# Performance work log

Hardware: AMD Instinct MI355X
Metric: run time of the kernel (lower is better)

## Reference

```python
import jax, jax.numpy as jnp
import numpy as np


def setup_inputs() -> dict:
    key = jax.random.key(0)
    k_x, k_q, k_k, k_v = jax.random.split(key, 4)
    seq_len, d_in, d_out = 4096, 1024, 1024
    x = jax.random.normal(k_x, (seq_len, d_in), dtype=jnp.float32)
    # torch nn.Linear weights are [d_out, d_in]; applied as x @ W.T
    scale = 1.0 / np.sqrt(d_in)
    Wq = jax.random.uniform(k_q, (d_out, d_in), jnp.float32, -scale, scale)
    Wk = jax.random.uniform(k_k, (d_out, d_in), jnp.float32, -scale, scale)
    Wv = jax.random.uniform(k_v, (d_out, d_in), jnp.float32, -scale, scale)
    return {"x": x, "Wq": Wq, "Wk": Wk, "Wv": Wv}


def reference(x, Wq, Wk, Wv):
    # x: [S, d_in]; Wq/Wk/Wv: [d_out, d_in]
    queries = x @ Wq.T          # [S, d_out]
    keys = x @ Wk.T             # [S, d_out]
    values = x @ Wv.T           # [S, d_out]
    d_k = keys.shape[-1]
    attn_scores = queries @ keys.T                      # [S, S]
    attn_weights = jax.nn.softmax(attn_scores / jnp.sqrt(jnp.float32(d_k)), axis=-1)
    S = attn_scores.shape[0]
    tril = jnp.tril(jnp.ones((S, S), dtype=attn_weights.dtype))
    masked = tril * attn_weights
    masked_norm = masked / jnp.sum(masked, axis=-1, keepdims=True)
    context_vec = masked_norm @ values                  # [S, d_out]
    return context_vec
```

## Files before the change

kernel.cpp:

```cpp
#include <hip/hip_runtime.h>
#include <hip/hip_bf16.h>


typedef __bf16 bf16_t;
typedef __bf16 bf16x4v __attribute__((ext_vector_type(4)));
typedef __bf16 bf16x8 __attribute__((ext_vector_type(8)));
typedef float f32x4 __attribute__((ext_vector_type(4)));
typedef unsigned char u8;
typedef long long i64_t;

#define AS1 __attribute__((address_space(1)))
#define AS3 __attribute__((address_space(3)))

__device__ __forceinline__ void async_copy16(const void* g, void* l) {
    __builtin_amdgcn_global_load_lds((AS1 void*)(g), (AS3 void*)(l), 16, 0, 0);
}

__device__ __forceinline__ u8 f32_to_fp8(float v) {
    return (u8)(__builtin_amdgcn_cvt_pk_fp8_f32(v, v, 0, false) & 0xff);
}

__device__ __forceinline__ void store_conv(float* p, float v) { *p = v; }
__device__ __forceinline__ void store_conv(bf16_t* p, float v) { *p = (bf16_t)v; }
__device__ __forceinline__ void store_conv(u8* p, float v) { *p = f32_to_fp8(v); }

__device__ __forceinline__ float sum64(const float* p) {
    const f32x4* v = (const f32x4*)p;
    float s = 0.f;
#pragma unroll
    for (int u = 0; u < 16; ++u) {
        f32x4 a = v[u];
        s += a[0] + a[1] + a[2] + a[3];
    }
    return s;
}

template <int EPI, typename OutT>
__device__ __forceinline__ void gemm_tile_bf16(const bf16_t* __restrict__ A, int lda,
                                               const bf16_t* __restrict__ B, int ldb,
                                               OutT* __restrict__ C, int ldc,
                                               int kb0, int kb1, float alpha,
                                               bf16_t* __restrict__ As,
                                               bf16_t* __restrict__ Bs,
                                               const float* __restrict__ inv) {
    constexpr int BK = 64;
    const int tid = threadIdx.x;
    const int lane = tid & 63, wave = tid >> 6;
    const int wm = wave >> 1, wn = wave & 1;
    const int q = lane >> 4, l16 = lane & 15;

    f32x4 acc[4][4] = {};

    const bf16_t* aSrc[4];
    const bf16_t* bSrc[4];
    int ldsOff[4];
#pragma unroll
    for (int it = 0; it < 4; ++it) {
        int c = it * 256 + tid;
        int r = c >> 3, b = c & 7;
        int sb = b ^ (r & 7);
        aSrc[it] = A + (size_t)r * lda + sb * 8;
        bSrc[it] = B + (size_t)r * ldb + sb * 8;
        ldsOff[it] = c * 8;
    }

    for (int kb = kb0; kb < kb1; ++kb) {
        const int k0 = kb * BK;
#pragma unroll
        for (int it = 0; it < 4; ++it) async_copy16(aSrc[it] + k0, &As[ldsOff[it]]);
#pragma unroll
        for (int it = 0; it < 4; ++it) async_copy16(bSrc[it] + k0, &Bs[ldsOff[it]]);
        __syncthreads();

#pragma unroll
        for (int k2 = 0; k2 < 2; ++k2) {
            bf16x8 af[4], bfr[4];
#pragma unroll
            for (int mt = 0; mt < 4; ++mt) {
                int m = wm * 64 + mt * 16 + l16;
                int blk = (k2 * 4 + q) ^ (m & 7);
                af[mt] = *(const bf16x8*)&As[m * BK + blk * 8];
            }
#pragma unroll
            for (int nt = 0; nt < 4; ++nt) {
                int nn = wn * 64 + nt * 16 + l16;
                int blk = (k2 * 4 + q) ^ (nn & 7);
                bfr[nt] = *(const bf16x8*)&Bs[nn * BK + blk * 8];
            }
#pragma unroll
            for (int mt = 0; mt < 4; ++mt)
#pragma unroll
                for (int nt = 0; nt < 4; ++nt)
                    acc[mt][nt] = __builtin_amdgcn_mfma_f32_16x16x32_bf16(
                        af[mt], bfr[nt], acc[mt][nt], 0, 0, 0);
        }
        __syncthreads();
    }

    const int row0 = wm * 64, col0 = wn * 64;
#pragma unroll
    for (int mt = 0; mt < 4; ++mt)
#pragma unroll
        for (int nt = 0; nt < 4; ++nt)
#pragma unroll
            for (int r = 0; r < 4; ++r) {
                int lr = row0 + mt * 16 + q * 4 + r;
                float v = acc[mt][nt][r];
                v = (EPI == 2) ? v * inv[lr] : v * alpha;
                store_conv(&C[(size_t)lr * ldc + col0 + nt * 16 + l16], v);
            }
}

__device__ __forceinline__ void scores_tile_fp8(const u8* __restrict__ A, int lda,
                                                const u8* __restrict__ B, int ldb,
                                                bf16_t* __restrict__ C, int ldc,
                                                float alpha,
                                                u8* __restrict__ As, u8* __restrict__ Bs,
                                                float* __restrict__ partial,
                                                int gr0, int gc0,
                                                float* __restrict__ sred) {
    const int tid = threadIdx.x;
    const int lane = tid & 63, wave = tid >> 6;
    const int wm = wave >> 1, wn = wave & 1;
    const int q = lane >> 4, l16 = lane & 15;

    f32x4 acc[4][2] = {};

    const u8* aSrc[4];
    int aOff[4];
#pragma unroll
    for (int it = 0; it < 4; ++it) {
        int c = it * 256 + tid;
        int r = c >> 3, b = c & 7;
        int sb = b ^ (r & 7);
        aSrc[it] = A + (size_t)r * lda + sb * 16;
        aOff[it] = c * 16;
    }
    const u8* bSrc[2];
    int bOff[2];
#pragma unroll
    for (int it = 0; it < 2; ++it) {
        int c = it * 256 + tid;
        int r = c >> 3, b = c & 7;
        int sb = b ^ (r & 7);
        bSrc[it] = B + (size_t)r * ldb + sb * 16;
        bOff[it] = c * 16;
    }

    for (int kb = 0; kb < 8; ++kb) {
        const int k0 = kb * 128;
#pragma unroll
        for (int it = 0; it < 4; ++it) async_copy16(aSrc[it] + k0, &As[aOff[it]]);
#pragma unroll
        for (int it = 0; it < 2; ++it) async_copy16(bSrc[it] + k0, &Bs[bOff[it]]);
        __syncthreads();

#pragma unroll
        for (int k2 = 0; k2 < 4; ++k2) {
            i64_t af[4], bfr[2];
            const int cb = 2 * k2 + (q >> 1), co = (q & 1) * 8;
#pragma unroll
            for (int mt = 0; mt < 4; ++mt) {
                int m = wm * 64 + mt * 16 + l16;
                af[mt] = *(const i64_t*)&As[m * 128 + ((cb ^ (m & 7)) << 4) + co];
            }
#pragma unroll
            for (int nt = 0; nt < 2; ++nt) {
                int nn = wn * 32 + nt * 16 + l16;
                bfr[nt] = *(const i64_t*)&Bs[nn * 128 + ((cb ^ (nn & 7)) << 4) + co];
            }
#pragma unroll
            for (int mt = 0; mt < 4; ++mt)
#pragma unroll
                for (int nt = 0; nt < 2; ++nt)
                    acc[mt][nt] = __builtin_amdgcn_mfma_f32_16x16x32_fp8_fp8(
                        af[mt], bfr[nt], acc[mt][nt], 0, 0, 0);
        }
        __syncthreads();
    }

    const int row0 = wm * 64, col0 = wn * 32;
    float esum[4][4];
#pragma unroll
    for (int mt = 0; mt < 4; ++mt)
#pragma unroll
        for (int r = 0; r < 4; ++r) esum[mt][r] = 0.f;
#pragma unroll
    for (int mt = 0; mt < 4; ++mt)
#pragma unroll
        for (int nt = 0; nt < 2; ++nt)
#pragma unroll
            for (int r = 0; r < 4; ++r) {
                int lr = row0 + mt * 16 + q * 4 + r;
                int lc = col0 + nt * 16 + l16;
                float p = (gc0 + lc > gr0 + lr) ? 0.f : __expf(acc[mt][nt][r] * alpha);
                esum[mt][r] += p;
                C[(size_t)lr * ldc + lc] = (bf16_t)p;
            }
#pragma unroll
    for (int mt = 0; mt < 4; ++mt)
#pragma unroll
        for (int r = 0; r < 4; ++r) {
#pragma unroll
            for (int off = 1; off < 16; off <<= 1)
                esum[mt][r] += __shfl_xor(esum[mt][r], off, 64);
            if (l16 == 0) sred[(row0 + mt * 16 + q * 4 + r) * 2 + wn] = esum[mt][r];
        }
    __syncthreads();
    if (tid < 128) partial[(size_t)tid * 64] = sred[tid * 2] + sred[tid * 2 + 1];
}

__global__ __launch_bounds__(256) void k_qkv(const bf16_t* __restrict__ xb,
                                             const bf16_t* __restrict__ wqk,
                                             const bf16_t* __restrict__ wvb,
                                             u8* __restrict__ qk,
                                             bf16_t* __restrict__ vt) {
    __shared__ __attribute__((aligned(16))) bf16_t As[128 * 64];
    __shared__ __attribute__((aligned(16))) bf16_t Bs[128 * 64];
    int b = blockIdx.x;
    if (b < 512) {
        int bmi = b & 3, bn = (b >> 2) & 15, bmo = b >> 6;
        int bm = bmo * 4 + bmi;
        gemm_tile_bf16<0, u8>(xb + (size_t)bm * 128 * 1024, 1024,
                              wqk + (size_t)bn * 128 * 1024, 1024,
                              qk + (size_t)bm * 128 * 2048 + bn * 128, 2048,
                              0, 16, 1.f, As, Bs, nullptr);
    } else {
        int t = b - 512;
        int bm = t & 7, bn = t >> 3;
        gemm_tile_bf16<0, bf16_t>(wvb + (size_t)bm * 128 * 1024, 1024,
                                  xb + (size_t)bn * 128 * 1024, 1024,
                                  vt + (size_t)bm * 128 * 4096 + bn * 128, 4096,
                                  0, 16, 1.f, As, Bs, nullptr);
    }
}

__global__ __launch_bounds__(256) void k_scores(const u8* __restrict__ qk,
                                                bf16_t* __restrict__ P,
                                                float* __restrict__ rowsum_part) {
    __shared__ __attribute__((aligned(16))) u8 As[128 * 128];
    __shared__ __attribute__((aligned(16))) u8 Bs[64 * 128];
    __shared__ float sred[128 * 2];
    int t = blockIdx.x;
    int bm = (int)((sqrtf(4.f * (float)t + 1.f) - 1.f) * 0.5f);
    while (bm * bm + bm > t) --bm;
    while ((bm + 1) * (bm + 1) + (bm + 1) <= t) ++bm;
    int bn = t - bm * bm - bm;
    scores_tile_fp8(qk + (size_t)bm * 128 * 2048, 2048,
                    qk + 1024 + (size_t)bn * 64 * 2048, 2048,
                    P + (size_t)bm * 128 * 4096 + bn * 64, 4096,
                    0.03125f, As, Bs,
                    rowsum_part + (size_t)bm * 128 * 64 + bn,
                    bm * 128, bn * 64, sred);
    if (bn == 2 * bm + 1) {
        float* rp = rowsum_part + (size_t)bm * 128 * 64;
        int tid = threadIdx.x;
        for (int r = tid >> 4; r < 128; r += 16)
            for (int u = 2 * bm + 2 + (tid & 15); u < 64; u += 16)
                rp[r * 64 + u] = 0.f;
    }
}

__global__ __launch_bounds__(256) void k_pv(const bf16_t* __restrict__ P,
                                            const bf16_t* __restrict__ vt,
                                            const float* __restrict__ rowsum_part,
                                            float* __restrict__ out,
                                            float* __restrict__ partials) {
    __shared__ __attribute__((aligned(16))) bf16_t As[128 * 64];
    __shared__ __attribute__((aligned(16))) bf16_t Bs[128 * 64];
    __shared__ float sInv[128];
    int b = blockIdx.x;
    int bn = b & 7, g = b >> 3;
    int bm, s, ns;
    if (g < 8)       { bm = g;                 s = 0;            ns = 1; }
    else if (g < 24) { bm = 8 + (g - 8) / 2;   s = (g - 8) % 2;  ns = 2; }
    else if (g < 48) { bm = 16 + (g - 24) / 3; s = (g - 24) % 3; ns = 3; }
    else             { bm = 24 + (g - 48) / 4; s = (g - 48) % 4; ns = 4; }
    int nk = 2 * (bm + 1);
    int kb0 = s * nk / ns;
    int kb1 = (s + 1) * nk / ns;

    const bf16_t* A = P + (size_t)bm * 128 * 4096;
    const bf16_t* B = vt + (size_t)bn * 128 * 4096;
    if (ns == 1) {
        int tid = threadIdx.x;
        if (tid < 128)
            sInv[tid] = 1.f / sum64(rowsum_part + (size_t)(bm * 128 + tid) * 64);
        gemm_tile_bf16<2, float>(A, 4096, B, 4096,
                                 out + (size_t)bm * 128 * 1024 + bn * 128, 1024,
                                 kb0, kb1, 1.f, As, Bs, sInv);
    } else {
        int cum = (bm < 16) ? (bm - 8) * 2
                : (bm < 24) ? 16 + (bm - 16) * 3
                            : 40 + (bm - 24) * 4;
        gemm_tile_bf16<0, float>(A, 4096, B, 4096,
                                 partials + ((size_t)(cum + s) * 8 + bn) * 16384, 128,
                                 kb0, kb1, 1.f, As, Bs, nullptr);
    }
}

__global__ __launch_bounds__(256) void k_reduce(const float* __restrict__ partials,
                                                const float* __restrict__ rowsum_part,
                                                float* __restrict__ out) {
    int b = blockIdx.x;
    int t = b % 192, p = b / 192;
    int bm = t % 24 + 8, bn = t / 24;
    int ns = (bm < 16) ? 2 : (bm < 24) ? 3 : 4;
    int cum = (bm < 16) ? (bm - 8) * 2
            : (bm < 24) ? 16 + (bm - 16) * 3
                        : 40 + (bm - 24) * 4;
    __shared__ float sInv[8];
    int tid = threadIdx.x;
    if (tid < 8) {
        int row = bm * 128 + p * 8 + tid;
        sInv[tid] = 1.f / sum64(rowsum_part + (size_t)row * 64);
    }
    __syncthreads();

    int idx = p * 1024 + tid * 4;
    int lr = idx >> 7, lc = idx & 127;
    float sx = 0.f, sy = 0.f, sz = 0.f, sw = 0.f;
    for (int u = 0; u < ns; ++u) {
        const float4 v = *(const float4*)(partials + ((size_t)(cum + u) * 8 + bn) * 16384 + idx);
        sx += v.x; sy += v.y; sz += v.z; sw += v.w;
    }
    float inv = sInv[lr - p * 8];
    float4 o = {sx * inv, sy * inv, sz * inv, sw * inv};
    *(float4*)(out + (size_t)(bm * 128 + lr) * 1024 + bn * 128 + lc) = o;
}

__global__ __launch_bounds__(256) void cast_to_bf16(const float* __restrict__ x,
                                                    const float* __restrict__ Wq,
                                                    const float* __restrict__ Wk,
                                                    const float* __restrict__ Wv,
                                                    bf16_t* __restrict__ xb,
                                                    bf16_t* __restrict__ wqk,
                                                    bf16_t* __restrict__ wv) {
    const int NX = (4096 * 1024) / 4;
    const int NW = (1024 * 1024) / 4;
    int idx = blockIdx.x * 256 + threadIdx.x;
    const float* src;
    bf16_t* dst;
    int off;
    if (idx < NX) {
        src = x; dst = xb; off = idx;
    } else if (idx < NX + NW) {
        src = Wq; dst = wqk; off = idx - NX;
    } else if (idx < NX + 2 * NW) {
        src = Wk; dst = wqk + (size_t)NW * 4; off = idx - NX - NW;
    } else {
        src = Wv; dst = wv; off = idx - NX - 2 * NW;
    }
    float4 f = ((const float4*)src)[off];
    bf16x4v o;
    o.x = (bf16_t)f.x; o.y = (bf16_t)f.y; o.z = (bf16_t)f.z; o.w = (bf16_t)f.w;
    *(bf16x4v*)(dst + (size_t)off * 4) = o;
}

extern "C" void kernel_launch(void* const* d_in, const int* in_sizes, int n_in,
                              void* d_out, int out_size, void* d_ws, size_t ws_size,
                              hipStream_t stream) {
    (void)in_sizes; (void)n_in; (void)out_size; (void)ws_size;
    const float* x  = (const float*)d_in[0];
    const float* Wq = (const float*)d_in[1];
    const float* Wk = (const float*)d_in[2];
    const float* Wv = (const float*)d_in[3];
    float* out = (float*)d_out;

    char* ws = (char*)d_ws;
    bf16_t* xb   = (bf16_t*)(ws + (size_t)0);
    bf16_t* wqk  = (bf16_t*)(ws + ((size_t)8 << 20));
    bf16_t* wvb  = (bf16_t*)(ws + ((size_t)12 << 20));
    u8*     qk   = (u8*)(ws + ((size_t)14 << 20));
    bf16_t* vt   = (bf16_t*)(ws + ((size_t)22 << 20));
    bf16_t* P    = (bf16_t*)(ws + ((size_t)30 << 20));
    float* rowsp = (float*)(ws + ((size_t)62 << 20));
    float* parts = (float*)(ws + ((size_t)64 << 20));

    cast_to_bf16<<<7168, 256, 0, stream>>>(x, Wq, Wk, Wv, xb, wqk, wvb);

    k_qkv<<<768, 256, 0, stream>>>(xb, wqk, wvb, qk, vt);

    k_scores<<<1056, 256, 0, stream>>>(qk, P, rowsp);

    k_pv<<<640, 256, 0, stream>>>(P, vt, rowsp, out, parts);
    k_reduce<<<3072, 256, 0, stream>>>(parts, rowsp, out);
}
```

Measured before the change: 198.2 us.

## Fuse split-K reduction into PV kernel via atomic last-block counters

Removes the separate k_reduce launch. The last-arriving split block for each output tile, detected with an atomic counter, sums the partials and applies the row normalization in place. The split-K schedule is also rebalanced to 1–6 splits over more row blocks, growing the grid from 640 to 816 blocks. Counters are zeroed in the cast kernel. The cost is an extra threadfence and atomic per block, plus a serialized reduction tail performed by a single block per tile.

```diff
diff --git a/kernel.cpp b/kernel.cpp
--- a/kernel.cpp
+++ b/kernel.cpp
@@ -265,68 +265,72 @@
                                             const bf16_t* __restrict__ vt,
                                             const float* __restrict__ rowsum_part,
                                             float* __restrict__ out,
-                                            float* __restrict__ partials) {
+                                            float* __restrict__ partials,
+                                            int* __restrict__ counters) {
     __shared__ __attribute__((aligned(16))) bf16_t As[128 * 64];
     __shared__ __attribute__((aligned(16))) bf16_t Bs[128 * 64];
     __shared__ float sInv[128];
+    __shared__ int lastFlag;
     int b = blockIdx.x;
     int bn = b & 7, g = b >> 3;
     int bm, s, ns;
-    if (g < 8)       { bm = g;                 s = 0;            ns = 1; }
-    else if (g < 24) { bm = 8 + (g - 8) / 2;   s = (g - 8) % 2;  ns = 2; }
-    else if (g < 48) { bm = 16 + (g - 24) / 3; s = (g - 24) % 3; ns = 3; }
-    else             { bm = 24 + (g - 48) / 4; s = (g - 48) % 4; ns = 4; }
+    if (g < 6)       { bm = g;                 s = 0;            ns = 1; }
+    else if (g < 18) { bm = 6 + (g - 6) / 2;   s = (g - 6) % 2;  ns = 2; }
+    else if (g < 36) { bm = 12 + (g - 18) / 3; s = (g - 18) % 3; ns = 3; }
+    else if (g < 60) { bm = 18 + (g - 36) / 4; s = (g - 36) % 4; ns = 4; }
+    else if (g < 90) { bm = 24 + (g - 60) / 5; s = (g - 60) % 5; ns = 5; }
+    else             { bm = 30 + (g - 90) / 6; s = (g - 90) % 6; ns = 6; }
     int nk = 2 * (bm + 1);
     int kb0 = s * nk / ns;
     int kb1 = (s + 1) * nk / ns;
+    int tid = threadIdx.x;
 
     const bf16_t* A = P + (size_t)bm * 128 * 4096;
     const bf16_t* B = vt + (size_t)bn * 128 * 4096;
     if (ns == 1) {
-        int tid = threadIdx.x;
         if (tid < 128)
             sInv[tid] = 1.f / sum64(rowsum_part + (size_t)(bm * 128 + tid) * 64);
         gemm_tile_bf16<2, float>(A, 4096, B, 4096,
                                  out + (size_t)bm * 128 * 1024 + bn * 128, 1024,
                                  kb0, kb1, 1.f, As, Bs, sInv);
-    } else {
-        int cum = (bm < 16) ? (bm - 8) * 2
-                : (bm < 24) ? 16 + (bm - 16) * 3
-                            : 40 + (bm - 24) * 4;
-        gemm_tile_bf16<0, float>(A, 4096, B, 4096,
-                                 partials + ((size_t)(cum + s) * 8 + bn) * 16384, 128,
-                                 kb0, kb1, 1.f, As, Bs, nullptr);
-    }
-}
-
-__global__ __launch_bounds__(256) void k_reduce(const float* __restrict__ partials,
-                                                const float* __restrict__ rowsum_part,
-                                                float* __restrict__ out) {
-    int b = blockIdx.x;
-    int t = b % 192, p = b / 192;
-    int bm = t % 24 + 8, bn = t / 24;
-    int ns = (bm < 16) ? 2 : (bm < 24) ? 3 : 4;
-    int cum = (bm < 16) ? (bm - 8) * 2
-            : (bm < 24) ? 16 + (bm - 16) * 3
-                        : 40 + (bm - 24) * 4;
-    __shared__ float sInv[8];
-    int tid = threadIdx.x;
-    if (tid < 8) {
-        int row = bm * 128 + p * 8 + tid;
-        sInv[tid] = 1.f / sum64(rowsum_part + (size_t)row * 64);
+        return;
+    }
+
+    int cum = (bm < 12) ? (bm - 6) * 2
+            : (bm < 18) ? 12 + (bm - 12) * 3
+            : (bm < 24) ? 30 + (bm - 18) * 4
+            : (bm < 30) ? 54 + (bm - 24) * 5
+                        : 84 + (bm - 30) * 6;
+    gemm_tile_bf16<0, float>(A, 4096, B, 4096,
+                             partials + ((size_t)(cum + s) * 8 + bn) * 16384, 128,
+                             kb0, kb1, 1.f, As, Bs, nullptr);
+
+    __threadfence();
+    if (tid == 0) {
+        int old = __hip_atomic_fetch_add(&counters[bm * 8 + bn], 1,
+                                         __ATOMIC_ACQ_REL, __HIP_MEMORY_SCOPE_AGENT);
+        lastFlag = (old == ns - 1);
     }
     __syncthreads();
-
-    int idx = p * 1024 + tid * 4;
-    int lr = idx >> 7, lc = idx & 127;
-    float sx = 0.f, sy = 0.f, sz = 0.f, sw = 0.f;
-    for (int u = 0; u < ns; ++u) {
-        const float4 v = *(const float4*)(partials + ((size_t)(cum + u) * 8 + bn) * 16384 + idx);
-        sx += v.x; sy += v.y; sz += v.z; sw += v.w;
-    }
-    float inv = sInv[lr - p * 8];
-    float4 o = {sx * inv, sy * inv, sz * inv, sw * inv};
-    *(float4*)(out + (size_t)(bm * 128 + lr) * 1024 + bn * 128 + lc) = o;
+    if (!lastFlag) return;
+    __threadfence();
+
+    if (tid < 128)
+        sInv[tid] = 1.f / sum64(rowsum_part + (size_t)(bm * 128 + tid) * 64);
+    __syncthreads();
+
+    const float* base = partials + (size_t)cum * 8 * 16384 + (size_t)bn * 16384;
+    for (int idx = tid * 4; idx < 16384; idx += 1024) {
+        float sx = 0.f, sy = 0.f, sz = 0.f, sw = 0.f;
+        for (int u = 0; u < ns; ++u) {
+            const float4 v = *(const float4*)(base + (size_t)u * 8 * 16384 + idx);
+            sx += v.x; sy += v.y; sz += v.z; sw += v.w;
+        }
+        int lr = idx >> 7, lc = idx & 127;
+        float inv = sInv[lr];
+        float4 o = {sx * inv, sy * inv, sz * inv, sw * inv};
+        *(float4*)(out + (size_t)(bm * 128 + lr) * 1024 + bn * 128 + lc) = o;
+    }
 }
 
 __global__ __launch_bounds__(256) void cast_to_bf16(const float* __restrict__ x,
@@ -335,10 +339,12 @@
                                                     const float* __restrict__ Wv,
                                                     bf16_t* __restrict__ xb,
                                                     bf16_t* __restrict__ wqk,
-                                                    bf16_t* __restrict__ wv) {
+                                                    bf16_t* __restrict__ wv,
+                                                    int* __restrict__ counters) {
     const int NX = (4096 * 1024) / 4;
     const int NW = (1024 * 1024) / 4;
     int idx = blockIdx.x * 256 + threadIdx.x;
+    if (blockIdx.x == 0) counters[threadIdx.x] = 0;
     const float* src;
     bf16_t* dst;
     int off;
@@ -375,14 +381,14 @@
     bf16_t* vt   = (bf16_t*)(ws + ((size_t)22 << 20));
     bf16_t* P    = (bf16_t*)(ws + ((size_t)30 << 20));
     float* rowsp = (float*)(ws + ((size_t)62 << 20));
+    int*   cnts  = (int*)(ws + ((size_t)63 << 20));
     float* parts = (float*)(ws + ((size_t)64 << 20));
 
-    cast_to_bf16<<<7168, 256, 0, stream>>>(x, Wq, Wk, Wv, xb, wqk, wvb);
+    cast_to_bf16<<<7168, 256, 0, stream>>>(x, Wq, Wk, Wv, xb, wqk, wvb, cnts);
 
     k_qkv<<<768, 256, 0, stream>>>(xb, wqk, wvb, qk, vt);
 
     k_scores<<<1056, 256, 0, stream>>>(qk, P, rowsp);
 
-    k_pv<<<640, 256, 0, stream>>>(P, vt, rowsp, out, parts);
-    k_reduce<<<3072, 256, 0, stream>>>(parts, rowsp, out);
-}
+    k_pv<<<816, 256, 0, stream>>>(P, vt, rowsp, out, parts, cnts);
+}
```

Result: slower. 382.9 us (+93.2%).

## Widen FP8 score tiles to 128x128 and overlap V projection with scores kernel

Applied to the files above, without the earlier changes.

The causal score kernel now uses 128x128 tiles instead of 128x64, so each wave computes a 64x64 sub-tile with twice as many MFMAs per LDS fragment load, and there are half as many row-sum partials per row (32 instead of 64). The V projection GEMM moves out of the QK projection kernel and into the same launch as the score tiles (256 V blocks plus 528 score blocks), so the two independent stages can share the GPU. In exchange, accumulator registers double, which may reduce occupancy, and diagonal tiles now waste more masked work.

```diff
diff --git a/kernel.cpp b/kernel.cpp
--- a/kernel.cpp
+++ b/kernel.cpp
@@ -24,11 +24,11 @@
 __device__ __forceinline__ void store_conv(bf16_t* p, float v) { *p = (bf16_t)v; }
 __device__ __forceinline__ void store_conv(u8* p, float v) { *p = f32_to_fp8(v); }
 
-__device__ __forceinline__ float sum64(const float* p) {
+__device__ __forceinline__ float sum32(const float* p) {
     const f32x4* v = (const f32x4*)p;
     float s = 0.f;
 #pragma unroll
-    for (int u = 0; u < 16; ++u) {
+    for (int u = 0; u < 8; ++u) {
         f32x4 a = v[u];
         s += a[0] + a[1] + a[2] + a[3];
     }
@@ -124,40 +124,32 @@
     const int wm = wave >> 1, wn = wave & 1;
     const int q = lane >> 4, l16 = lane & 15;
 
-    f32x4 acc[4][2] = {};
+    f32x4 acc[4][4] = {};
 
     const u8* aSrc[4];
-    int aOff[4];
+    const u8* bSrc[4];
+    int ldsOff[4];
 #pragma unroll
     for (int it = 0; it < 4; ++it) {
         int c = it * 256 + tid;
         int r = c >> 3, b = c & 7;
         int sb = b ^ (r & 7);
         aSrc[it] = A + (size_t)r * lda + sb * 16;
-        aOff[it] = c * 16;
-    }
-    const u8* bSrc[2];
-    int bOff[2];
-#pragma unroll
-    for (int it = 0; it < 2; ++it) {
-        int c = it * 256 + tid;
-        int r = c >> 3, b = c & 7;
-        int sb = b ^ (r & 7);
         bSrc[it] = B + (size_t)r * ldb + sb * 16;
-        bOff[it] = c * 16;
+        ldsOff[it] = c * 16;
     }
 
     for (int kb = 0; kb < 8; ++kb) {
         const int k0 = kb * 128;
 #pragma unroll
-        for (int it = 0; it < 4; ++it) async_copy16(aSrc[it] + k0, &As[aOff[it]]);
-#pragma unroll
-        for (int it = 0; it < 2; ++it) async_copy16(bSrc[it] + k0, &Bs[bOff[it]]);
+        for (int it = 0; it < 4; ++it) async_copy16(aSrc[it] + k0, &As[ldsOff[it]]);
+#pragma unroll
+        for (int it = 0; it < 4; ++it) async_copy16(bSrc[it] + k0, &Bs[ldsOff[it]]);
         __syncthreads();
 
 #pragma unroll
         for (int k2 = 0; k2 < 4; ++k2) {
-            i64_t af[4], bfr[2];
+            i64_t af[4], bfr[4];
             const int cb = 2 * k2 + (q >> 1), co = (q & 1) * 8;
 #pragma unroll
             for (int mt = 0; mt < 4; ++mt) {
@@ -165,21 +157,21 @@
                 af[mt] = *(const i64_t*)&As[m * 128 + ((cb ^ (m & 7)) << 4) + co];
             }
 #pragma unroll
-            for (int nt = 0; nt < 2; ++nt) {
-                int nn = wn * 32 + nt * 16 + l16;
+            for (int nt = 0; nt < 4; ++nt) {
+                int nn = wn * 64 + nt * 16 + l16;
                 bfr[nt] = *(const i64_t*)&Bs[nn * 128 + ((cb ^ (nn & 7)) << 4) + co];
             }
 #pragma unroll
             for (int mt = 0; mt < 4; ++mt)
 #pragma unroll
-                for (int nt = 0; nt < 2; ++nt)
+                for (int nt = 0; nt < 4; ++nt)
                     acc[mt][nt] = __builtin_amdgcn_mfma_f32_16x16x32_fp8_fp8(
                         af[mt], bfr[nt], acc[mt][nt], 0, 0, 0);
         }
         __syncthreads();
     }
 
-    const int row0 = wm * 64, col0 = wn * 32;
+    const int row0 = wm * 64, col0 = wn * 64;
     float esum[4][4];
 #pragma unroll
     for (int mt = 0; mt < 4; ++mt)
@@ -188,7 +180,7 @@
 #pragma unroll
     for (int mt = 0; mt < 4; ++mt)
 #pragma unroll
-        for (int nt = 0; nt < 2; ++nt)
+        for (int nt = 0; nt < 4; ++nt)
 #pragma unroll
             for (int r = 0; r < 4; ++r) {
                 int lr = row0 + mt * 16 + q * 4 + r;
@@ -207,57 +199,60 @@
             if (l16 == 0) sred[(row0 + mt * 16 + q * 4 + r) * 2 + wn] = esum[mt][r];
         }
     __syncthreads();
-    if (tid < 128) partial[(size_t)tid * 64] = sred[tid * 2] + sred[tid * 2 + 1];
+    if (tid < 128) partial[(size_t)tid * 32] = sred[tid * 2] + sred[tid * 2 + 1];
 }
 
 __global__ __launch_bounds__(256) void k_qkv(const bf16_t* __restrict__ xb,
                                              const bf16_t* __restrict__ wqk,
-                                             const bf16_t* __restrict__ wvb,
-                                             u8* __restrict__ qk,
-                                             bf16_t* __restrict__ vt) {
+                                             u8* __restrict__ qk) {
     __shared__ __attribute__((aligned(16))) bf16_t As[128 * 64];
     __shared__ __attribute__((aligned(16))) bf16_t Bs[128 * 64];
     int b = blockIdx.x;
-    if (b < 512) {
-        int bmi = b & 3, bn = (b >> 2) & 15, bmo = b >> 6;
-        int bm = bmo * 4 + bmi;
-        gemm_tile_bf16<0, u8>(xb + (size_t)bm * 128 * 1024, 1024,
-                              wqk + (size_t)bn * 128 * 1024, 1024,
-                              qk + (size_t)bm * 128 * 2048 + bn * 128, 2048,
-                              0, 16, 1.f, As, Bs, nullptr);
-    } else {
-        int t = b - 512;
-        int bm = t & 7, bn = t >> 3;
+    int bm = b & 31, bn = b >> 5;
+    gemm_tile_bf16<0, u8>(xb + (size_t)bm * 128 * 1024, 1024,
+                          wqk + (size_t)bn * 128 * 1024, 1024,
+                          qk + (size_t)bm * 128 * 2048 + bn * 128, 2048,
+                          0, 16, 1.f, As, Bs, nullptr);
+}
+
+__global__ __launch_bounds__(256) void k_sv(const bf16_t* __restrict__ xb,
+                                            const bf16_t* __restrict__ wvb,
+                                            const u8* __restrict__ qk,
+                                            bf16_t* __restrict__ vt,
+                                            bf16_t* __restrict__ P,
+                                            float* __restrict__ rowsum_part) {
+    __shared__ __attribute__((aligned(16))) char smem[33 * 1024 + 1024];
+    int b = blockIdx.x;
+    if (b < 256) {
+        bf16_t* As = (bf16_t*)smem;
+        bf16_t* Bs = (bf16_t*)(smem + 16384);
+        int bm = b & 7, bn = b >> 3;
         gemm_tile_bf16<0, bf16_t>(wvb + (size_t)bm * 128 * 1024, 1024,
                                   xb + (size_t)bn * 128 * 1024, 1024,
                                   vt + (size_t)bm * 128 * 4096 + bn * 128, 4096,
                                   0, 16, 1.f, As, Bs, nullptr);
-    }
-}
-
-__global__ __launch_bounds__(256) void k_scores(const u8* __restrict__ qk,
-                                                bf16_t* __restrict__ P,
-                                                float* __restrict__ rowsum_part) {
-    __shared__ __attribute__((aligned(16))) u8 As[128 * 128];
-    __shared__ __attribute__((aligned(16))) u8 Bs[64 * 128];
-    __shared__ float sred[128 * 2];
-    int t = blockIdx.x;
-    int bm = (int)((sqrtf(4.f * (float)t + 1.f) - 1.f) * 0.5f);
-    while (bm * bm + bm > t) --bm;
-    while ((bm + 1) * (bm + 1) + (bm + 1) <= t) ++bm;
-    int bn = t - bm * bm - bm;
+        return;
+    }
+    u8* As = (u8*)smem;
+    u8* Bs = (u8*)(smem + 16384);
+    float* sred = (float*)(smem + 32768);
+    int t = b - 256;
+    int bm = (int)((sqrtf(8.f * (float)t + 1.f) - 1.f) * 0.5f);
+    while (bm * (bm + 1) / 2 > t) --bm;
+    while ((bm + 1) * (bm + 2) / 2 <= t) ++bm;
+    int bn = t - bm * (bm + 1) / 2;
     scores_tile_fp8(qk + (size_t)bm * 128 * 2048, 2048,
-                    qk + 1024 + (size_t)bn * 64 * 2048, 2048,
-                    P + (size_t)bm * 128 * 4096 + bn * 64, 4096,
+                    qk + 1024 + (size_t)bn * 128 * 2048, 2048,
+                    P + (size_t)bm * 128 * 4096 + bn * 128, 4096,
                     0.03125f, As, Bs,
-                    rowsum_part + (size_t)bm * 128 * 64 + bn,
-                    bm * 128, bn * 64, sred);
-    if (bn == 2 * bm + 1) {
-        float* rp = rowsum_part + (size_t)bm * 128 * 64;
+                    rowsum_part + (size_t)bm * 128 * 32 + bn,
+                    bm * 128, bn * 128, sred);
+    if (bn == bm) {
+        float* rp = rowsum_part + (size_t)bm * 128 * 32;
         int tid = threadIdx.x;
         for (int r = tid >> 4; r < 128; r += 16)
-            for (int u = 2 * bm + 2 + (tid & 15); u < 64; u += 16)
-                rp[r * 64 + u] = 0.f;
+            for (int u = bm + 1 + (tid & 15); u < 32; u += 16)
+                rp[r * 32 + u] = 0.f;
     }
 }
 
@@ -285,7 +280,7 @@
     if (ns == 1) {
         int tid = threadIdx.x;
         if (tid < 128)
-            sInv[tid] = 1.f / sum64(rowsum_part + (size_t)(bm * 128 + tid) * 64);
+            sInv[tid] = 1.f / sum32(rowsum_part + (size_t)(bm * 128 + tid) * 32);
         gemm_tile_bf16<2, float>(A, 4096, B, 4096,
                                  out + (size_t)bm * 128 * 1024 + bn * 128, 1024,
                                  kb0, kb1, 1.f, As, Bs, sInv);
@@ -313,7 +308,7 @@
     int tid = threadIdx.x;
     if (tid < 8) {
         int row = bm * 128 + p * 8 + tid;
-        sInv[tid] = 1.f / sum64(rowsum_part + (size_t)row * 64);
+        sInv[tid] = 1.f / sum32(rowsum_part + (size_t)row * 32);
     }
     __syncthreads();
 
@@ -379,9 +374,9 @@
 
     cast_to_bf16<<<7168, 256, 0, stream>>>(x, Wq, Wk, Wv, xb, wqk, wvb);
 
-    k_qkv<<<768, 256, 0, stream>>>(xb, wqk, wvb, qk, vt);
-
-    k_scores<<<1056, 256, 0, stream>>>(qk, P, rowsp);
+    k_qkv<<<512, 256, 0, stream>>>(xb, wqk, qk);
+
+    k_sv<<<784, 256, 0, stream>>>(xb, wvb, qk, vt, P, rowsp);
 
     k_pv<<<640, 256, 0, stream>>>(P, vt, rowsp, out, parts);
     k_reduce<<<3072, 256, 0, stream>>>(parts, rowsp, out);
```

After: 189.2 us. 4.5% less time.
